# Kernel tuning notes

Hardware: AMD Instinct MI355X
Metric: run time of the kernel (lower is better)

The kernel has to match this reference:

```python
import jax, jax.numpy as jnp
import numpy as np

B, CH, S = 1024, 60, 288
F1, D, F2, NCLS, KL = 8, 2, 16, 4, 64
BN_EPS = 1e-3
PD_EPS = 1e-6  # torch.nn.PairwiseDistance default eps


def _conv(x, w, pad_w=0, groups=1):
    return jax.lax.conv_general_dilated(
        x, w, window_strides=(1, 1), padding=[(0, 0), (pad_w, pad_w)],
        dimension_numbers=("NCHW", "OIHW", "NCHW"), feature_group_count=groups)


def _bn(x, g, b, m, v):
    # eval-mode BatchNorm2d with running stats, eps=0.001
    inv = g / jnp.sqrt(v + BN_EPS)
    return x * inv[None, :, None, None] + (b - m * inv)[None, :, None, None]


def _avgpool_w(x, k):
    s = jax.lax.reduce_window(x, 0.0, jax.lax.add, (1, 1, 1, k), (1, 1, 1, k), "VALID")
    return s / k


def setup_inputs() -> dict:
    key = jax.random.key(0)
    ks = jax.random.split(key, 16)
    x = jax.random.normal(ks[0], (B, 1, CH, S), jnp.float32)
    y = jax.random.randint(ks[1], (B,), 0, NCLS, dtype=jnp.int32)
    conv1_w = jax.random.normal(ks[2], (F1, 1, 1, KL), jnp.float32) * 0.05
    dw = jax.random.normal(ks[3], (F1 * D, 1, CH, 1), jnp.float32) * 0.2
    # Conv2dWithConstraint: torch.renorm(w, p=2, dim=0, maxnorm=1) applied to .data
    norms = jnp.sqrt(jnp.sum(dw * dw, axis=(1, 2, 3), keepdims=True))
    dw_w = dw * jnp.minimum(1.0, 1.0 / jnp.maximum(norms, 1e-7))
    pw_w = jax.random.normal(ks[4], (F2, F1 * D, 1, 1), jnp.float32) * 0.1
    fc_w = jax.random.normal(ks[5], (NCLS, 144), jnp.float32) * 0.05
    fc_b = jnp.zeros((NCLS,), jnp.float32)

    def bnp(k, c):
        k1, k2, k3, k4 = jax.random.split(k, 4)
        g = 1.0 + 0.1 * jax.random.normal(k1, (c,), jnp.float32)
        b = 0.1 * jax.random.normal(k2, (c,), jnp.float32)
        m = 0.1 * jax.random.normal(k3, (c,), jnp.float32)
        v = jax.random.uniform(k4, (c,), jnp.float32, 0.5, 1.5)
        return g, b, m, v

    bn1_g, bn1_b, bn1_m, bn1_v = bnp(ks[6], F1)
    bn2_g, bn2_b, bn2_m, bn2_v = bnp(ks[7], F1 * D)
    bn3_g, bn3_b, bn3_m, bn3_v = bnp(ks[8], F2)
    return dict(x=x, y=y, conv1_w=conv1_w,
                bn1_g=bn1_g, bn1_b=bn1_b, bn1_m=bn1_m, bn1_v=bn1_v,
                dw_w=dw_w, bn2_g=bn2_g, bn2_b=bn2_b, bn2_m=bn2_m, bn2_v=bn2_v,
                pw_w=pw_w, bn3_g=bn3_g, bn3_b=bn3_b, bn3_m=bn3_m, bn3_v=bn3_v,
                fc_w=fc_w, fc_b=fc_b)


def _centroid_loss(feat, y):
    # per-class mean (torch code computes it from detached numpy -> stop_gradient)
    sums = jax.ops.segment_sum(feat, y, num_segments=NCLS)       # [NCLS, 144]
    cnts = jax.ops.segment_sum(jnp.ones((feat.shape[0],), feat.dtype), y, num_segments=NCLS)
    cent = jax.lax.stop_gradient(sums / jnp.maximum(cnts, 1.0)[:, None])
    diff = feat - cent[y] + PD_EPS                                # [B, 144]
    dist = jnp.sqrt(jnp.sum(diff * diff, axis=-1))                # [B]
    return jnp.mean(dist)


def reference(x, y, conv1_w, bn1_g, bn1_b, bn1_m, bn1_v,
              dw_w, bn2_g, bn2_b, bn2_m, bn2_v,
              pw_w, bn3_g, bn3_b, bn3_m, bn3_v, fc_w, fc_b):
    h = _conv(x, conv1_w, pad_w=KL // 2)                 # [B, F1, 60, 289]
    h = _bn(h, bn1_g, bn1_b, bn1_m, bn1_v)
    h = _conv(h, dw_w, pad_w=0, groups=F1)               # [B, F1*D, 1, 289]
    h = _bn(h, bn2_g, bn2_b, bn2_m, bn2_v)
    h = jax.nn.elu(h)
    h = _avgpool_w(h, 4)                                 # width 72 (dropout = eval no-op)
    h = _conv(h, pw_w)                                   # [B, F2, 1, 72]
    h = _bn(h, bn3_g, bn3_b, bn3_m, bn3_v)
    h = jax.nn.elu(h)
    h = _avgpool_w(h, 8)                                 # width 9
    feat = h.reshape(h.shape[0], -1)                     # [B, 144]
    cl = _centroid_loss(feat, y)
    probs = jax.nn.softmax(feat @ fc_w.T + fc_b, axis=1)
    return probs, cl
```

## Files before the change

kernel.cpp:

```cpp
#include <hip/hip_runtime.h>
#include <math.h>

#define NB   1024
#define CH   60
#define SW   288
#define F1C  8
#define FD   16
#define F2C  16
#define KLEN 64
#define NCLS 4
#define NV   9
#define FEAT 144
#define NTHR 320
#define NREP 4

#define XR_STRIDE 356
#define PH_STRIDE 76
#define W1_STRIDE 68

__device__ __forceinline__ float elu1(float v) {
    return v > 0.f ? v : __expf(v) - 1.f;
}

__global__ __launch_bounds__(NTHR, 5) void eegnet_fwd(
    const float* __restrict__ x, const int* __restrict__ y,
    const float* __restrict__ conv1_w,
    const float* __restrict__ bn1_g, const float* __restrict__ bn1_b,
    const float* __restrict__ bn1_m, const float* __restrict__ bn1_v,
    const float* __restrict__ dw_w,
    const float* __restrict__ bn2_g, const float* __restrict__ bn2_b,
    const float* __restrict__ bn2_m, const float* __restrict__ bn2_v,
    const float* __restrict__ pw_w,
    const float* __restrict__ bn3_g, const float* __restrict__ bn3_b,
    const float* __restrict__ bn3_m, const float* __restrict__ bn3_v,
    const float* __restrict__ fc_w, const float* __restrict__ fc_b,
    float* __restrict__ probs_out, float* __restrict__ feat_out,
    float* __restrict__ sums, int* __restrict__ cnt)
{
    __shared__ __align__(16) float s_xr[FD * XR_STRIDE];
    __shared__ __align__(16) float s_w1[F1C * W1_STRIDE];
    __shared__ __align__(16) float s_ph[FD * PH_STRIDE];
    __shared__ float s_pwT[FD * F2C];
    __shared__ float s_feat[FEAT];
    __shared__ float s_A[FD], s_Cb[FD], s_a3[F2C], s_c3[F2C];

    const int tid = threadIdx.x;
    const int b = blockIdx.x;

    if (tid == 0) atomicAdd(&cnt[(b & (NREP - 1)) * NCLS + y[b]], 1);
    for (int i = tid; i < F1C * KLEN; i += NTHR)
        s_w1[(i >> 6) * W1_STRIDE + (i & 63)] = conv1_w[i];
    for (int i = tid; i < F2C * FD; i += NTHR)
        s_pwT[(i & 15) * F2C + (i >> 4)] = pw_w[i];
    for (int i = tid; i < FD * 68; i += NTHR) {
        int f = i / 68, p = i % 68;
        int wp = (p < 32) ? p : (288 + p);
        s_xr[f * XR_STRIDE + wp] = 0.f;
    }
    if (tid < FD) {
        const int f = tid, f1 = f >> 1;
        const float inv1 = bn1_g[f1] / sqrtf(bn1_v[f1] + 1e-3f);
        const float c1 = bn1_b[f1] - bn1_m[f1] * inv1;
        const float inv2 = bn2_g[f] / sqrtf(bn2_v[f] + 1e-3f);
        const float c2 = bn2_b[f] - bn2_m[f] * inv2;
        float sdw = 0.f;
        for (int ch = 0; ch < CH; ++ch) sdw += dw_w[f * CH + ch];
        s_A[f] = inv2 * inv1;
        s_Cb[f] = inv2 * c1 * sdw + c2;
        const float inv3 = bn3_g[f] / sqrtf(bn3_v[f] + 1e-3f);
        s_a3[f] = inv3;
        s_c3[f] = bn3_b[f] - bn3_m[f] * inv3;
    }

    if (tid < SW) {
        const float* xp = x + (size_t)b * (CH * SW) + tid;
        float acc[FD];
        #pragma unroll
        for (int f = 0; f < FD; ++f) acc[f] = 0.f;
        float v[30];
        #pragma unroll
        for (int j = 0; j < 30; ++j) v[j] = xp[j * SW];
        #pragma unroll
        for (int j = 0; j < 30; ++j) {
            const float xv = v[j];
            #pragma unroll
            for (int f = 0; f < FD; ++f)
                acc[f] = fmaf(dw_w[f * CH + j], xv, acc[f]);
        }
        #pragma unroll
        for (int j = 0; j < 30; ++j) v[j] = xp[(30 + j) * SW];
        #pragma unroll
        for (int j = 0; j < 30; ++j) {
            const float xv = v[j];
            #pragma unroll
            for (int f = 0; f < FD; ++f)
                acc[f] = fmaf(dw_w[f * CH + 30 + j], xv, acc[f]);
        }
        #pragma unroll
        for (int f = 0; f < FD; ++f) s_xr[f * XR_STRIDE + 32 + tid] = acc[f];
    }
    __syncthreads();

    if (tid < 288) {
        const int f = tid & 15;
        const int q = tid >> 4;
        const float4* xp = (const float4*)&s_xr[f * XR_STRIDE + 16 * q];
        const float4* wp = (const float4*)&s_w1[(f >> 1) * W1_STRIDE];
        float cw[20];
        #pragma unroll
        for (int i = 0; i < 4; ++i) {
            const float4 t = xp[i];
            cw[4*i] = t.x; cw[4*i+1] = t.y; cw[4*i+2] = t.z; cw[4*i+3] = t.w;
        }
        float bb[16];
        #pragma unroll
        for (int j = 0; j < 16; ++j) bb[j] = 0.f;
        #pragma unroll
        for (int m = 0; m < 16; ++m) {
            {
                const float4 t = xp[m + 4];
                const int s = (4 * (m + 4)) % 20;
                cw[s] = t.x; cw[s+1] = t.y; cw[s+2] = t.z; cw[s+3] = t.w;
            }
            const float4 wv = wp[m];
            #pragma unroll
            for (int j = 0; j < 16; ++j) {
                bb[j] = fmaf(wv.x, cw[(4*m + j    ) % 20], bb[j]);
                bb[j] = fmaf(wv.y, cw[(4*m + j + 1) % 20], bb[j]);
                bb[j] = fmaf(wv.z, cw[(4*m + j + 2) % 20], bb[j]);
                bb[j] = fmaf(wv.w, cw[(4*m + j + 3) % 20], bb[j]);
            }
        }
        const float Af = s_A[f], Cf = s_Cb[f];
        float e[16];
        #pragma unroll
        for (int j = 0; j < 16; ++j) e[j] = elu1(fmaf(Af, bb[j], Cf));
        float4 ph;
        ph.x = (e[0]  + e[1]  + e[2]  + e[3])  * 0.25f;
        ph.y = (e[4]  + e[5]  + e[6]  + e[7])  * 0.25f;
        ph.z = (e[8]  + e[9]  + e[10] + e[11]) * 0.25f;
        ph.w = (e[12] + e[13] + e[14] + e[15]) * 0.25f;
        *(float4*)&s_ph[f * PH_STRIDE + 4 * q] = ph;
    }
    __syncthreads();

    if (tid < FEAT) {
        const int f2 = tid / NV;
        const int v = tid - f2 * NV;
        float su[8];
        #pragma unroll
        for (int k = 0; k < 8; ++k) su[k] = 0.f;
        #pragma unroll
        for (int f = 0; f < FD; ++f) {
            const float w = s_pwT[f * F2C + f2];
            const float4 p0 = *(const float4*)&s_ph[f * PH_STRIDE + 8 * v];
            const float4 p1 = *(const float4*)&s_ph[f * PH_STRIDE + 8 * v + 4];
            su[0] = fmaf(w, p0.x, su[0]); su[1] = fmaf(w, p0.y, su[1]);
            su[2] = fmaf(w, p0.z, su[2]); su[3] = fmaf(w, p0.w, su[3]);
            su[4] = fmaf(w, p1.x, su[4]); su[5] = fmaf(w, p1.y, su[5]);
            su[6] = fmaf(w, p1.z, su[6]); su[7] = fmaf(w, p1.w, su[7]);
        }
        const float a3f = s_a3[f2], c3f = s_c3[f2];
        float acc = 0.f;
        #pragma unroll
        for (int k = 0; k < 8; ++k) acc += elu1(fmaf(a3f, su[k], c3f));
        const float ft = acc * 0.125f;
        s_feat[tid] = ft;
        feat_out[(size_t)b * FEAT + tid] = ft;
        atomicAdd(&sums[((b & (NREP - 1)) * NCLS + y[b]) * FEAT + tid], ft);
    }
    __syncthreads();

    if (tid < 64) {
        float lg0 = 0.f, lg1 = 0.f, lg2 = 0.f, lg3 = 0.f;
        for (int j = tid; j < FEAT; j += 64) {
            const float fv = s_feat[j];
            lg0 = fmaf(fv, fc_w[0 * FEAT + j], lg0);
            lg1 = fmaf(fv, fc_w[1 * FEAT + j], lg1);
            lg2 = fmaf(fv, fc_w[2 * FEAT + j], lg2);
            lg3 = fmaf(fv, fc_w[3 * FEAT + j], lg3);
        }
        #pragma unroll
        for (int off = 32; off > 0; off >>= 1) {
            lg0 += __shfl_down(lg0, off, 64);
            lg1 += __shfl_down(lg1, off, 64);
            lg2 += __shfl_down(lg2, off, 64);
            lg3 += __shfl_down(lg3, off, 64);
        }
        if (tid == 0) {
            lg0 += fc_b[0]; lg1 += fc_b[1]; lg2 += fc_b[2]; lg3 += fc_b[3];
            const float m = fmaxf(fmaxf(lg0, lg1), fmaxf(lg2, lg3));
            const float e0 = __expf(lg0 - m), e1 = __expf(lg1 - m);
            const float e2 = __expf(lg2 - m), e3 = __expf(lg3 - m);
            const float inv = 1.f / (e0 + e1 + e2 + e3);
            float* po = probs_out + (size_t)b * NCLS;
            po[0] = e0 * inv; po[1] = e1 * inv; po[2] = e2 * inv; po[3] = e3 * inv;
        }
    }
}

__global__ __launch_bounds__(64) void eegnet_dist(
    const float* __restrict__ feat, const int* __restrict__ y,
    const float* __restrict__ sums, const int* __restrict__ cnt,
    float* __restrict__ cl_out)
{
    __shared__ float s_cent[NCLS * FEAT];
    const int tid = threadIdx.x;
    for (int i = tid; i < NCLS * FEAT; i += 64) {
        const int c = i / FEAT;
        const float sm = sums[(0 * NCLS + c) * FEAT + (i - c * FEAT)]
                       + sums[(1 * NCLS + c) * FEAT + (i - c * FEAT)]
                       + sums[(2 * NCLS + c) * FEAT + (i - c * FEAT)]
                       + sums[(3 * NCLS + c) * FEAT + (i - c * FEAT)];
        const float cf = (float)(cnt[0 * NCLS + c] + cnt[1 * NCLS + c]
                               + cnt[2 * NCLS + c] + cnt[3 * NCLS + c]);
        s_cent[i] = sm / fmaxf(cf, 1.0f);
    }
    __syncthreads();

    const int s = blockIdx.x * 64 + tid;
    const float* fp = feat + (size_t)s * FEAT;
    const float* cp = &s_cent[y[s] * FEAT];
    float acc = 0.f;
    #pragma unroll
    for (int j = 0; j < FEAT; j += 4) {
        const float4 fv = *reinterpret_cast<const float4*>(fp + j);
        float d;
        d = fv.x - cp[j + 0] + 1e-6f; acc = fmaf(d, d, acc);
        d = fv.y - cp[j + 1] + 1e-6f; acc = fmaf(d, d, acc);
        d = fv.z - cp[j + 2] + 1e-6f; acc = fmaf(d, d, acc);
        d = fv.w - cp[j + 3] + 1e-6f; acc = fmaf(d, d, acc);
    }
    float dist = sqrtf(acc);
    #pragma unroll
    for (int off = 32; off > 0; off >>= 1) dist += __shfl_down(dist, off, 64);
    if (tid == 0) atomicAdd(cl_out, dist * (1.0f / 1024.0f));
}

extern "C" void kernel_launch(void* const* d_in, const int* in_sizes, int n_in,
                              void* d_out, int out_size, void* d_ws, size_t ws_size,
                              hipStream_t stream) {
    const float* x       = (const float*)d_in[0];
    const int*   y       = (const int*)d_in[1];
    const float* conv1_w = (const float*)d_in[2];
    const float* bn1_g   = (const float*)d_in[3];
    const float* bn1_b   = (const float*)d_in[4];
    const float* bn1_m   = (const float*)d_in[5];
    const float* bn1_v   = (const float*)d_in[6];
    const float* dw_w    = (const float*)d_in[7];
    const float* bn2_g   = (const float*)d_in[8];
    const float* bn2_b   = (const float*)d_in[9];
    const float* bn2_m   = (const float*)d_in[10];
    const float* bn2_v   = (const float*)d_in[11];
    const float* pw_w    = (const float*)d_in[12];
    const float* bn3_g   = (const float*)d_in[13];
    const float* bn3_b   = (const float*)d_in[14];
    const float* bn3_m   = (const float*)d_in[15];
    const float* bn3_v   = (const float*)d_in[16];
    const float* fc_w    = (const float*)d_in[17];
    const float* fc_b    = (const float*)d_in[18];

    float* out   = (float*)d_out;
    float* probs = out;
    float* cl    = out + 4096;
    char*  ws    = (char*)d_ws;
    float* sums  = (float*)ws;
    int*   cnt   = (int*)(ws + 9216);
    float* feat  = (float*)(ws + 9280);

    hipMemsetAsync(ws, 0, 9280, stream);
    hipMemsetAsync(cl, 0, sizeof(float), stream);
    eegnet_fwd<<<NB, NTHR, 0, stream>>>(
        x, y, conv1_w, bn1_g, bn1_b, bn1_m, bn1_v,
        dw_w, bn2_g, bn2_b, bn2_m, bn2_v,
        pw_w, bn3_g, bn3_b, bn3_m, bn3_v,
        fc_w, fc_b, probs, feat, sums, cnt);
    eegnet_dist<<<16, 64, 0, stream>>>(feat, y, sums, cnt, cl);
}
```

Before: 55.04 us.

## Stage input channels through shared memory with float4 loads, raise occupancy hint

The depthwise channel reduction now loads the input in chunks of six channels, using float4 loads from all 320 threads into a shared buffer, instead of each of 288 threads holding 30 scalar loads in registers. This is meant to coalesce and vectorize global reads and cut register pressure, so the launch bound's waves-per-unit hint goes from 5 to 8. In exchange it adds ten chunk iterations with two block barriers each, and there is less in-flight memory parallelism per thread. The distance kernel also gets a small index cleanup.

```diff
diff --git a/kernel.cpp b/kernel.cpp
--- a/kernel.cpp
+++ b/kernel.cpp
@@ -13,6 +13,7 @@
 #define FEAT 144
 #define NTHR 320
 #define NREP 4
+#define XCH  6
 
 #define XR_STRIDE 356
 #define PH_STRIDE 76
@@ -22,7 +23,7 @@
     return v > 0.f ? v : __expf(v) - 1.f;
 }
 
-__global__ __launch_bounds__(NTHR, 5) void eegnet_fwd(
+__global__ __launch_bounds__(NTHR, 8) void eegnet_fwd(
     const float* __restrict__ x, const int* __restrict__ y,
     const float* __restrict__ conv1_w,
     const float* __restrict__ bn1_g, const float* __restrict__ bn1_b,
@@ -37,6 +38,7 @@
     float* __restrict__ probs_out, float* __restrict__ feat_out,
     float* __restrict__ sums, int* __restrict__ cnt)
 {
+    __shared__ __align__(16) float s_x[XCH * SW];
     __shared__ __align__(16) float s_xr[FD * XR_STRIDE];
     __shared__ __align__(16) float s_w1[F1C * W1_STRIDE];
     __shared__ __align__(16) float s_ph[FD * PH_STRIDE];
@@ -72,32 +74,33 @@
         s_c3[f] = bn3_b[f] - bn3_m[f] * inv3;
     }
 
-    if (tid < SW) {
-        const float* xp = x + (size_t)b * (CH * SW) + tid;
+    {
+        const float4* xb4 = (const float4*)(x + (size_t)b * (CH * SW));
+        float4* sx4 = (float4*)s_x;
         float acc[FD];
         #pragma unroll
         for (int f = 0; f < FD; ++f) acc[f] = 0.f;
-        float v[30];
-        #pragma unroll
-        for (int j = 0; j < 30; ++j) v[j] = xp[j * SW];
-        #pragma unroll
-        for (int j = 0; j < 30; ++j) {
-            const float xv = v[j];
+        #pragma unroll
+        for (int c0 = 0; c0 < CH; c0 += XCH) {
+            const float4* src = xb4 + c0 * 72;
+            sx4[tid] = src[tid];
+            if (tid < 432 - NTHR) sx4[tid + NTHR] = src[tid + NTHR];
+            __syncthreads();
+            if (tid < SW) {
+                #pragma unroll
+                for (int r = 0; r < XCH; ++r) {
+                    const float xv = s_x[r * SW + tid];
+                    #pragma unroll
+                    for (int f = 0; f < FD; ++f)
+                        acc[f] = fmaf(dw_w[f * CH + c0 + r], xv, acc[f]);
+                }
+            }
+            __syncthreads();
+        }
+        if (tid < SW) {
             #pragma unroll
-            for (int f = 0; f < FD; ++f)
-                acc[f] = fmaf(dw_w[f * CH + j], xv, acc[f]);
-        }
-        #pragma unroll
-        for (int j = 0; j < 30; ++j) v[j] = xp[(30 + j) * SW];
-        #pragma unroll
-        for (int j = 0; j < 30; ++j) {
-            const float xv = v[j];
-            #pragma unroll
-            for (int f = 0; f < FD; ++f)
-                acc[f] = fmaf(dw_w[f * CH + 30 + j], xv, acc[f]);
-        }
-        #pragma unroll
-        for (int f = 0; f < FD; ++f) s_xr[f * XR_STRIDE + 32 + tid] = acc[f];
+            for (int f = 0; f < FD; ++f) s_xr[f * XR_STRIDE + 32 + tid] = acc[f];
+        }
     }
     __syncthreads();
 
@@ -208,10 +211,11 @@
     const int tid = threadIdx.x;
     for (int i = tid; i < NCLS * FEAT; i += 64) {
         const int c = i / FEAT;
-        const float sm = sums[(0 * NCLS + c) * FEAT + (i - c * FEAT)]
-                       + sums[(1 * NCLS + c) * FEAT + (i - c * FEAT)]
-                       + sums[(2 * NCLS + c) * FEAT + (i - c * FEAT)]
-                       + sums[(3 * NCLS + c) * FEAT + (i - c * FEAT)];
+        const int j = i - c * FEAT;
+        const float sm = sums[(0 * NCLS + c) * FEAT + j]
+                       + sums[(1 * NCLS + c) * FEAT + j]
+                       + sums[(2 * NCLS + c) * FEAT + j]
+                       + sums[(3 * NCLS + c) * FEAT + j];
         const float cf = (float)(cnt[0 * NCLS + c] + cnt[1 * NCLS + c]
                                + cnt[2 * NCLS + c] + cnt[3 * NCLS + c]);
         s_cent[i] = sm / fmaxf(cf, 1.0f);
```

Result: slower. 81.53 us (+48.1%).
